# Performance work log

Measured on AMD Instinct MI355X. Metric: run time of the kernel, lower is better.

## Reference

```python
import jax, jax.numpy as jnp
import numpy as np

# Real spherical-harmonic polynomial constants (l=0..3), Cartesian form
C0 = 0.28209479177387814
C1 = 0.4886025119029199
C2_XY = 1.0925484305920792
C2_0 = 0.31539156525252005
C2_2 = 0.5462742152960396
C3_3 = 0.5900435899266435
C3_2 = 2.890611442640554
C3_1 = 0.4570457994644658
C3_0 = 0.3731763325901154
C3_P2 = 1.445305721320277


def spherical_harmonics(x):
    # x: [B, N, 3] -> dict l -> [B, N, 2l+1]
    px, py, pz = x[..., 0], x[..., 1], x[..., 2]
    x2, y2, z2 = px * px, py * py, pz * pz
    Y0 = C0 * jnp.ones(px.shape + (1,), dtype=x.dtype)
    Y1 = C1 * jnp.stack([py, pz, px], axis=-1)
    Y2 = jnp.stack([
        C2_XY * px * py,
        C2_XY * py * pz,
        C2_0 * (2.0 * z2 - x2 - y2),
        C2_XY * px * pz,
        C2_2 * (x2 - y2),
    ], axis=-1)
    Y3 = jnp.stack([
        C3_3 * py * (3.0 * x2 - y2),
        C3_2 * px * py * pz,
        C3_1 * py * (4.0 * z2 - x2 - y2),
        C3_0 * pz * (2.0 * z2 - 3.0 * x2 - 3.0 * y2),
        C3_1 * px * (4.0 * z2 - x2 - y2),
        C3_P2 * pz * (x2 - y2),
        C3_3 * px * (x2 - 3.0 * y2),
    ], axis=-1)
    return {0: Y0, 1: Y1, 2: Y2, 3: Y3}


def zernike_monoms(x, max_deg=3):
    # Per-degree Zernike monomials: multiply SH of degree l by powers of |x|^2
    # keeping total degree 2d+l <= max_deg. Returns dict l -> [B, N, 2l+1, c_l]
    m = max_deg // 2  # = 1
    n2 = jnp.sum(x * x, axis=-1)  # [B, N]
    Y = spherical_harmonics(x)
    p = [jnp.ones_like(n2), n2]  # |x|^0, |x|^2
    z = {}
    for l, Yl in Y.items():
        chans = [p[d][..., None] * Yl for d in range(m + 1) if 2 * d + l <= max_deg]
        z[l] = jnp.stack(chans, axis=-1)  # [B, N, 2l+1, c_l]
    return z


def setup_inputs() -> dict:
    key = jax.random.key(0)
    k = jax.random.split(key, 6)
    x = jax.random.normal(k[0], (32, 32768, 3), dtype=jnp.float32)
    W0 = jax.random.normal(k[1], (2, 4), dtype=jnp.float32) * 0.5
    b0 = jax.random.normal(k[2], (4,), dtype=jnp.float32) * 0.1
    W1 = jax.random.normal(k[3], (2, 4), dtype=jnp.float32) * 0.5
    W2 = jax.random.normal(k[4], (1, 4), dtype=jnp.float32) * 0.5
    W3 = jax.random.normal(k[5], (1, 4), dtype=jnp.float32) * 0.5
    return {"x": x, "W0": W0, "b0": b0, "W1": W1, "W2": W2, "W3": W3}


def reference(x, W0, b0, W1, W2, W3):
    z = zernike_monoms(x, 3)
    # Per-degree Dense interwiners (units=4); l=0 has bias, l>0 bias-free.
    y0 = jnp.einsum('bnmc,cu->bnmu', z[0], W0) + b0  # [B,N,1,4]
    y1 = jnp.einsum('bnmc,cu->bnmu', z[1], W1)       # [B,N,3,4]
    y2 = jnp.einsum('bnmc,cu->bnmu', z[2], W2)       # [B,N,5,4]
    y3 = jnp.einsum('bnmc,cu->bnmu', z[3], W3)       # [B,N,7,4]
    # concat_types: concat along the spherical (axis=-2) dim -> [B,N,16,4]
    return jnp.concatenate([y0, y1, y2, y3], axis=-2)
```

## Files before the change

kernel.cpp:

```cpp
#include <hip/hip_runtime.h>


typedef float f32x4 __attribute__((ext_vector_type(4)));

#define C0f   0.28209479177387814f
#define C1f   0.4886025119029199f
#define C2XYf 1.0925484305920792f
#define C20f  0.31539156525252005f
#define C22f  0.5462742152960396f
#define C33f  0.5900435899266435f
#define C32f  2.890611442640554f
#define C31f  0.4570457994644658f
#define C30f  0.3731763325901154f
#define C3P2f 1.445305721320277f

#define PTS_PER_BLOCK 256
#define REC 24

__global__ __launch_bounds__(256) void zernike_fused(
    const float* __restrict__ x,
    const float* __restrict__ W0, const float* __restrict__ b0,
    const float* __restrict__ W1, const float* __restrict__ W2,
    const float* __restrict__ W3,
    f32x4* __restrict__ out, int npoints)
{
    __shared__ float sm[PTS_PER_BLOCK * REC];

    const int tid   = threadIdx.x;
    const int pbase = blockIdx.x * PTS_PER_BLOCK;

    float a0[4], a1[4], g10[4], g11[4], w2r[4], w3r[4];
#pragma unroll
    for (int u = 0; u < 4; ++u) {
        a0[u]  = C0f * W0[u] + b0[u];
        a1[u]  = C0f * W0[4 + u];
        g10[u] = W1[u];
        g11[u] = W1[4 + u];
        w2r[u] = W2[u];
        w3r[u] = W3[u];
    }

    {
        const int p = pbase + tid;
        if (p < npoints) {
            const float px = x[3 * p + 0];
            const float py = x[3 * p + 1];
            const float pz = x[3 * p + 2];
            const float x2 = px * px, y2 = py * py, z2 = pz * pz;
            const float n2 = x2 + y2 + z2;

            float* rec = &sm[tid * REC];

            f32x4 G0, G1;
            G0.x = fmaf(n2, a1[0], a0[0]);   G0.y = fmaf(n2, a1[1], a0[1]);
            G0.z = fmaf(n2, a1[2], a0[2]);   G0.w = fmaf(n2, a1[3], a0[3]);
            G1.x = fmaf(n2, g11[0], g10[0]); G1.y = fmaf(n2, g11[1], g10[1]);
            G1.z = fmaf(n2, g11[2], g10[2]); G1.w = fmaf(n2, g11[3], g10[3]);
            *(f32x4*)(rec + 0) = G0;
            *(f32x4*)(rec + 4) = G1;

            rec[8]  = 1.0f;
            rec[9]  = C1f * py;
            rec[10] = C1f * pz;
            rec[11] = C1f * px;
            rec[12] = C2XYf * px * py;
            rec[13] = C2XYf * py * pz;
            rec[14] = C20f * (2.0f * z2 - x2 - y2);
            rec[15] = C2XYf * px * pz;
            rec[16] = C22f * (x2 - y2);
            rec[17] = C33f * py * (3.0f * x2 - y2);
            rec[18] = C32f * px * py * pz;
            rec[19] = C31f * py * (4.0f * z2 - x2 - y2);
            rec[20] = C30f * pz * (2.0f * z2 - 3.0f * x2 - 3.0f * y2);
            rec[21] = C31f * px * (4.0f * z2 - x2 - y2);
            rec[22] = C3P2f * pz * (x2 - y2);
            rec[23] = C33f * px * (x2 - 3.0f * y2);
        }
    }
    __syncthreads();

    const int plb = tid >> 4;
    const int m   = tid & 15;

    const bool useG = (m < 4);
    const int  goff = (m == 0) ? 0 : 4;
    f32x4 wreg;
    {
        const int sel = (m < 9) ? 0 : 1;
        wreg.x = sel ? w3r[0] : w2r[0];
        wreg.y = sel ? w3r[1] : w2r[1];
        wreg.z = sel ? w3r[2] : w2r[2];
        wreg.w = sel ? w3r[3] : w2r[3];
    }

    const float* rec0 = &sm[plb * REC];
    f32x4* op = out + (size_t)blockIdx.x * (PTS_PER_BLOCK * 16) + tid;

#pragma unroll
    for (int k = 0; k < 16; ++k) {
        const float* rec = rec0 + k * (16 * REC);
        const float  s   = rec[8 + m];
        const f32x4  g   = *(const f32x4*)(rec + goff);

        f32x4 r;
        r.x = s * (useG ? g.x : wreg.x);
        r.y = s * (useG ? g.y : wreg.y);
        r.z = s * (useG ? g.z : wreg.z);
        r.w = s * (useG ? g.w : wreg.w);

        op[k * 256] = r;
    }
}

extern "C" void kernel_launch(void* const* d_in, const int* in_sizes, int n_in,
                              void* d_out, int out_size, void* d_ws, size_t ws_size,
                              hipStream_t stream) {
    const float* x  = (const float*)d_in[0];
    const float* W0 = (const float*)d_in[1];
    const float* b0 = (const float*)d_in[2];
    const float* W1 = (const float*)d_in[3];
    const float* W2 = (const float*)d_in[4];
    const float* W3 = (const float*)d_in[5];

    const int npoints = in_sizes[0] / 3;
    const int blocks  = (npoints + PTS_PER_BLOCK - 1) / PTS_PER_BLOCK;

    zernike_fused<<<blocks, 256, 0, stream>>>(
        x, W0, b0, W1, W2, W3, (f32x4*)d_out, npoints);
}
```

Measured before the change: 49.22 us.

## Make each wave own its LDS slice and loop over tiles with prefetched inputs

Each block now handles four 256-point tiles. Each wave writes and reads only its own 64-point slice of shared memory, so the block-wide barrier becomes a per-wave LDS wait. The next tile's coordinates are loaded while the current tile is being stored, and LDS records are written as vector stores. This hides global load latency and cuts synchronisation, at the cost of four times fewer blocks and a possible loss of occupancy across the GPU.

```diff
diff --git a/kernel.cpp b/kernel.cpp
--- a/kernel.cpp
+++ b/kernel.cpp
@@ -14,8 +14,9 @@
 #define C30f  0.3731763325901154f
 #define C3P2f 1.445305721320277f
 
-#define PTS_PER_BLOCK 256
-#define REC 24
+#define PTS   256
+#define REC   24
+#define TILES 4
 
 __global__ __launch_bounds__(256) void zernike_fused(
     const float* __restrict__ x,
@@ -24,10 +25,11 @@
     const float* __restrict__ W3,
     f32x4* __restrict__ out, int npoints)
 {
-    __shared__ float sm[PTS_PER_BLOCK * REC];
+    __shared__ float sm[PTS * REC];
 
-    const int tid   = threadIdx.x;
-    const int pbase = blockIdx.x * PTS_PER_BLOCK;
+    const int tid  = threadIdx.x;
+    const int wave = tid >> 6;
+    const int lane = tid & 63;
 
     float a0[4], a1[4], g10[4], g11[4], w2r[4], w3r[4];
 #pragma unroll
@@ -40,48 +42,10 @@
         w3r[u] = W3[u];
     }
 
-    {
-        const int p = pbase + tid;
-        if (p < npoints) {
-            const float px = x[3 * p + 0];
-            const float py = x[3 * p + 1];
-            const float pz = x[3 * p + 2];
-            const float x2 = px * px, y2 = py * py, z2 = pz * pz;
-            const float n2 = x2 + y2 + z2;
+    float* wbuf = &sm[(wave * 64) * REC];
 
-            float* rec = &sm[tid * REC];
-
-            f32x4 G0, G1;
-            G0.x = fmaf(n2, a1[0], a0[0]);   G0.y = fmaf(n2, a1[1], a0[1]);
-            G0.z = fmaf(n2, a1[2], a0[2]);   G0.w = fmaf(n2, a1[3], a0[3]);
-            G1.x = fmaf(n2, g11[0], g10[0]); G1.y = fmaf(n2, g11[1], g10[1]);
-            G1.z = fmaf(n2, g11[2], g10[2]); G1.w = fmaf(n2, g11[3], g10[3]);
-            *(f32x4*)(rec + 0) = G0;
-            *(f32x4*)(rec + 4) = G1;
-
-            rec[8]  = 1.0f;
-            rec[9]  = C1f * py;
-            rec[10] = C1f * pz;
-            rec[11] = C1f * px;
-            rec[12] = C2XYf * px * py;
-            rec[13] = C2XYf * py * pz;
-            rec[14] = C20f * (2.0f * z2 - x2 - y2);
-            rec[15] = C2XYf * px * pz;
-            rec[16] = C22f * (x2 - y2);
-            rec[17] = C33f * py * (3.0f * x2 - y2);
-            rec[18] = C32f * px * py * pz;
-            rec[19] = C31f * py * (4.0f * z2 - x2 - y2);
-            rec[20] = C30f * pz * (2.0f * z2 - 3.0f * x2 - 3.0f * y2);
-            rec[21] = C31f * px * (4.0f * z2 - x2 - y2);
-            rec[22] = C3P2f * pz * (x2 - y2);
-            rec[23] = C33f * px * (x2 - 3.0f * y2);
-        }
-    }
-    __syncthreads();
-
-    const int plb = tid >> 4;
-    const int m   = tid & 15;
-
+    const int  m    = lane & 15;
+    const int  qrow = lane >> 4;
     const bool useG = (m < 4);
     const int  goff = (m == 0) ? 0 : 4;
     f32x4 wreg;
@@ -93,22 +57,93 @@
         wreg.w = sel ? w3r[3] : w2r[3];
     }
 
-    const float* rec0 = &sm[plb * REC];
-    f32x4* op = out + (size_t)blockIdx.x * (PTS_PER_BLOCK * 16) + tid;
+    const int tile0 = blockIdx.x * TILES;
 
+    float px, py, pz;
+    {
+        const int p  = tile0 * PTS + wave * 64 + lane;
+        const int pc = p < npoints ? p : 0;
+        px = x[3 * pc + 0]; py = x[3 * pc + 1]; pz = x[3 * pc + 2];
+    }
+
+    for (int t = 0; t < TILES; ++t) {
+        const int tbase = (tile0 + t) * PTS;
+        if (tbase >= npoints) break;
+
+        __builtin_amdgcn_sched_barrier(0);
+
+        {
+            const float x2 = px * px, y2 = py * py, z2 = pz * pz;
+            const float n2 = x2 + y2 + z2;
+            float* rec = &wbuf[lane * REC];
+
+            f32x4 G0, G1, S0, S1, S2, S3;
+            G0.x = fmaf(n2, a1[0], a0[0]);   G0.y = fmaf(n2, a1[1], a0[1]);
+            G0.z = fmaf(n2, a1[2], a0[2]);   G0.w = fmaf(n2, a1[3], a0[3]);
+            G1.x = fmaf(n2, g11[0], g10[0]); G1.y = fmaf(n2, g11[1], g10[1]);
+            G1.z = fmaf(n2, g11[2], g10[2]); G1.w = fmaf(n2, g11[3], g10[3]);
+            S0 = f32x4{1.0f, C1f * py, C1f * pz, C1f * px};
+            S1 = f32x4{C2XYf * px * py,
+                       C2XYf * py * pz,
+                       C20f * (2.0f * z2 - x2 - y2),
+                       C2XYf * px * pz};
+            S2 = f32x4{C22f * (x2 - y2),
+                       C33f * py * (3.0f * x2 - y2),
+                       C32f * px * py * pz,
+                       C31f * py * (4.0f * z2 - x2 - y2)};
+            S3 = f32x4{C30f * pz * (2.0f * z2 - 3.0f * x2 - 3.0f * y2),
+                       C31f * px * (4.0f * z2 - x2 - y2),
+                       C3P2f * pz * (x2 - y2),
+                       C33f * px * (x2 - 3.0f * y2)};
+            *(f32x4*)(rec + 0)  = G0;
+            *(f32x4*)(rec + 4)  = G1;
+            *(f32x4*)(rec + 8)  = S0;
+            *(f32x4*)(rec + 12) = S1;
+            *(f32x4*)(rec + 16) = S2;
+            *(f32x4*)(rec + 20) = S3;
+        }
+
+        if (t + 1 < TILES) {
+            const int p  = (tile0 + t + 1) * PTS + wave * 64 + lane;
+            const int pc = p < npoints ? p : 0;
+            px = x[3 * pc + 0]; py = x[3 * pc + 1]; pz = x[3 * pc + 2];
+        }
+
+        asm volatile("s_waitcnt lgkmcnt(0)" ::: "memory");
+        __builtin_amdgcn_sched_barrier(0);
+
+        f32x4* op = out + (size_t)(tbase + wave * 64) * 16 + lane;
+
+        if (tbase + PTS <= npoints) {
 #pragma unroll
-    for (int k = 0; k < 16; ++k) {
-        const float* rec = rec0 + k * (16 * REC);
-        const float  s   = rec[8 + m];
-        const f32x4  g   = *(const f32x4*)(rec + goff);
-
-        f32x4 r;
-        r.x = s * (useG ? g.x : wreg.x);
-        r.y = s * (useG ? g.y : wreg.y);
-        r.z = s * (useG ? g.z : wreg.z);
-        r.w = s * (useG ? g.w : wreg.w);
-
-        op[k * 256] = r;
+            for (int k = 0; k < 16; ++k) {
+                const float* rec = &wbuf[(k * 4 + qrow) * REC];
+                const float  s   = rec[8 + m];
+                const f32x4  g   = *(const f32x4*)(rec + goff);
+                f32x4 r;
+                r.x = s * (useG ? g.x : wreg.x);
+                r.y = s * (useG ? g.y : wreg.y);
+                r.z = s * (useG ? g.z : wreg.z);
+                r.w = s * (useG ? g.w : wreg.w);
+                op[k * 64] = r;
+            }
+        } else {
+            const int lim = (npoints - tbase - wave * 64) * 16;
+#pragma unroll
+            for (int k = 0; k < 16; ++k) {
+                if (k * 64 + lane < lim) {
+                    const float* rec = &wbuf[(k * 4 + qrow) * REC];
+                    const float  s   = rec[8 + m];
+                    const f32x4  g   = *(const f32x4*)(rec + goff);
+                    f32x4 r;
+                    r.x = s * (useG ? g.x : wreg.x);
+                    r.y = s * (useG ? g.y : wreg.y);
+                    r.z = s * (useG ? g.z : wreg.z);
+                    r.w = s * (useG ? g.w : wreg.w);
+                    op[k * 64] = r;
+                }
+            }
+        }
     }
 }
 
@@ -123,7 +158,8 @@
     const float* W3 = (const float*)d_in[5];
 
     const int npoints = in_sizes[0] / 3;
-    const int blocks  = (npoints + PTS_PER_BLOCK - 1) / PTS_PER_BLOCK;
+    const int per_blk = PTS * TILES;
+    const int blocks  = (npoints + per_blk - 1) / per_blk;
 
     zernike_fused<<<blocks, 256, 0, stream>>>(
         x, W0, b0, W1, W2, W3, (f32x4*)d_out, npoints);
```

Measured after the change: 49.20 us. Within noise of the previous version (-0.0%).
